# Performance work log

Hardware: AMD Instinct MI355X
Metric: run time of the kernel (lower is better)

Reference implementation:

```python
import jax, jax.numpy as jnp
import numpy as np

B, P, K = 32, 1024, 16  # clouds, points per cloud, neighbors


def setup_inputs() -> dict:
    key = jax.random.key(0)
    ks = jax.random.split(key, 5)
    N, C, H, D = B * P, 64, 128, 3
    x = jax.random.normal(ks[0], (N, C), dtype=jnp.float32)
    pos = jax.random.normal(ks[1], (N, D), dtype=jnp.float32)
    batch = jnp.arange(N, dtype=jnp.int64) // P  # cloud id per node
    W_e = jax.random.normal(ks[2], (2 * C, H), dtype=jnp.float32) * 0.05
    b_e = jnp.zeros((H,), dtype=jnp.float32)
    W_sc = jax.random.normal(ks[3], (C, H), dtype=jnp.float32) * 0.05
    b_sc = jnp.zeros((H,), dtype=jnp.float32)
    return {"x": x, "pos": pos, "batch": batch,
            "W_e": W_e, "b_e": b_e, "W_sc": W_sc, "b_sc": b_sc}


def _knn_idx(posb):
    # posb: [B, P, D] -> idx [B, P, K]: K nearest neighbors (sources) per target node,
    # within each cloud, excluding self (loop=False in torch_geometric.knn_graph).
    sq = jnp.sum(posb * posb, axis=-1)                       # [B, P]
    d2 = sq[:, :, None] + sq[:, None, :] - 2.0 * jnp.einsum('bid,bjd->bij', posb, posb)
    d2 = d2 + jnp.eye(P, dtype=posb.dtype)[None] * jnp.finfo(posb.dtype).max / 2
    _, idx = jax.lax.top_k(-d2, K)                           # [B, P, K]
    return idx


def reference(x, pos, batch, W_e, b_e, W_sc, b_sc):
    C = x.shape[-1]
    xb = x.reshape(B, P, C)
    posb = pos.reshape(B, P, -1)
    idx = _knn_idx(posb)                                     # [B, P, K]
    # gather neighbor (source) features per target node
    x_j = jax.vmap(lambda xc, ic: xc[ic])(xb, idx)           # [B, P, K, C]
    x_i = xb[:, :, None, :]                                  # [B, P, 1, C]
    # EdgeConv message: nn([x_i, x_j - x_i]), here Linear + ReLU
    e = jnp.concatenate([jnp.broadcast_to(x_i, x_j.shape), x_j - x_i], axis=-1)  # [B,P,K,2C]
    msg = jax.nn.relu(jnp.einsum('bpke,eh->bpkh', e, W_e) + b_e)
    agg = jnp.max(msg, axis=2)                               # max aggregation -> [B, P, H]
    shortcut = x @ W_sc + b_sc                               # [N, H]
    out = agg.reshape(-1, agg.shape[-1]) + shortcut
    return out
```

## Files before the change

kernel.cpp:

```cpp
#include <hip/hip_runtime.h>
#include <float.h>
#include <stdint.h>

#define BATCHES 32
#define P 1024
#define KNN 16
#define C 64
#define H 128
#define N (BATCHES * P)
#define SPLITS 8
#define CPS 128
#define QB 32
#define PADH 136

typedef short short8 __attribute__((ext_vector_type(8)));
typedef float floatx4 __attribute__((ext_vector_type(4)));

struct alignas(16) F4 { float x, y, z, w; };

__device__ __forceinline__ unsigned short f2bf(float f) {
    unsigned u = __float_as_uint(f);
    unsigned r = (u + 0x7FFF + ((u >> 16) & 1)) >> 16;
    return (unsigned short)r;
}

__global__ __launch_bounds__(256) void prep_kernel(
    const float* __restrict__ W_e, const float* __restrict__ b_e,
    const float* __restrict__ W_sc, const float* __restrict__ b_sc,
    const float* __restrict__ X,
    unsigned short* __restrict__ WT, float* __restrict__ bias,
    unsigned short* __restrict__ V)
{
    __shared__ unsigned short Vs[128][PADH];
    __shared__ unsigned short Wb[128 * 64];
    int b = blockIdx.x;
    int t = threadIdx.x;
    if (b < 96) {
        int i = b * 256 + t;
        int col = i >> 6, c = i & 63;
        float w;
        if (col < 128)      w = W_e[c * 128 + col] - W_e[(64 + c) * 128 + col];
        else if (col < 256) w = W_e[(64 + c) * 128 + (col - 128)];
        else                w = W_sc[c * 128 + (col - 256)];
        WT[col * 64 + c] = f2bf(w);
        if (c == 0) {
            bias[col] = (col < 128) ? b_e[col] : (col < 256 ? 0.0f : b_sc[col - 256]);
        }
        return;
    }

    int vb = b - 96;
    int m0 = vb * 128;
    int w  = t >> 6, ln = t & 63;
    int lm = ln & 15, kg = ln >> 4;

#pragma unroll 8
    for (int i = 0; i < 32; ++i) {
        int m = i * 256 + t;
        int k = m >> 7, h = m & 127;
        Wb[h * 64 + ((k + 8 * h) & 63)] = f2bf(W_e[(size_t)(64 + k) * 128 + h]);
    }

    short8 a0[2], a1[2];
#pragma unroll
    for (int i = 0; i < 2; ++i) {
        int row = m0 + (2 * w + i) * 16 + lm;
        const float4* ar = (const float4*)(X + (size_t)row * 64 + kg * 8);
        float4 f0 = ar[0], f1 = ar[1], f2 = ar[8], f3 = ar[9];
        a0[i][0] = (short)f2bf(f0.x); a0[i][1] = (short)f2bf(f0.y);
        a0[i][2] = (short)f2bf(f0.z); a0[i][3] = (short)f2bf(f0.w);
        a0[i][4] = (short)f2bf(f1.x); a0[i][5] = (short)f2bf(f1.y);
        a0[i][6] = (short)f2bf(f1.z); a0[i][7] = (short)f2bf(f1.w);
        a1[i][0] = (short)f2bf(f2.x); a1[i][1] = (short)f2bf(f2.y);
        a1[i][2] = (short)f2bf(f2.z); a1[i][3] = (short)f2bf(f2.w);
        a1[i][4] = (short)f2bf(f3.x); a1[i][5] = (short)f2bf(f3.y);
        a1[i][6] = (short)f2bf(f3.z); a1[i][7] = (short)f2bf(f3.w);
    }
    __syncthreads();

#pragma unroll 2
    for (int ct = 0; ct < 8; ++ct) {
        int col = ct * 16 + lm;
        int sbase = col * 64;
        short8 b0 = *(const short8*)&Wb[sbase + ((8 * (kg + col)) & 63)];
        short8 b1 = *(const short8*)&Wb[sbase + ((8 * (kg + col) + 32) & 63)];
#pragma unroll
        for (int i = 0; i < 2; ++i) {
            floatx4 acc = {0.0f, 0.0f, 0.0f, 0.0f};
            acc = __builtin_amdgcn_mfma_f32_16x16x32_bf16(a0[i], b0, acc, 0, 0, 0);
            acc = __builtin_amdgcn_mfma_f32_16x16x32_bf16(a1[i], b1, acc, 0, 0, 0);
#pragma unroll
            for (int r = 0; r < 4; ++r)
                Vs[(2 * w + i) * 16 + kg * 4 + r][col] = f2bf(acc[r]);
        }
    }
    __syncthreads();

    uint2* Vg = (uint2*)V + (size_t)vb * 4096;
#pragma unroll
    for (int i = t; i < 4096; i += 256) {
        int row = i >> 5, off = (i & 31) * 4;
        Vg[i] = *(const uint2*)&Vs[row][off];
    }
}

struct SM {
    F4 spos[P + 8];
    union {
        struct {
            float lists[SPLITS][16][QB];
            unsigned short offs[SPLITS][QB];
            unsigned short cnts[SPLITS][QB];
            float Tq[QB];
        };
        struct {
            unsigned short Ubuf[QB][PADH];
            unsigned short Sbuf[QB][PADH];
        };
    };
    int nbr[QB][KNN];
};

__global__ __launch_bounds__(256, 4) void knn_gemm_kernel(
    const float* __restrict__ pos, const float* __restrict__ X,
    const unsigned short* __restrict__ WT, const float* __restrict__ bias,
    const unsigned short* __restrict__ V,
    float* __restrict__ out)
{
    __shared__ __align__(16) SM A;

    int t = threadIdx.x;
    int q = t & 31, s = t >> 5;
    int blk = blockIdx.x;
    int batch = blk >> 5;
    int qblk  = blk & 31;
    int iloc  = qblk * QB + q;
    int so    = qblk >> 2;
    bool wave_owns = ((t >> 6) == (so >> 1));

    const float* pb = pos + (size_t)batch * P * 3;
    for (int j = t; j < P; j += 256) {
        float x = pb[j * 3 + 0], y = pb[j * 3 + 1], z = pb[j * 3 + 2];
        float sq = __fadd_rn(__fadd_rn(__fmul_rn(x, x), __fmul_rn(y, y)),
                             __fmul_rn(z, z));
        A.spos[j] = F4{x, y, z, sq};
    }
    __syncthreads();

    F4 me = A.spos[iloc];
    const int j0 = s * CPS;

    float d[16];
#pragma unroll
    for (int k = 0; k < 16; ++k) d[k] = FLT_MAX;

    auto dist_nc = [&](const F4& c) -> float {
        float dot = __fadd_rn(__fadd_rn(__fmul_rn(me.x, c.x), __fmul_rn(me.y, c.y)),
                              __fmul_rn(me.z, c.z));
        return __fadd_rn(__fadd_rn(me.w, c.w), __fmul_rn(-2.0f, dot));
    };
    auto dist = [&](const F4& c, int j) -> float {
        float d2 = dist_nc(c);
        return (j == iloc) ? FLT_MAX : d2;
    };
    auto insert = [&](float d2) {
#pragma unroll
        for (int k = 15; k >= 1; --k)
            d[k] = __builtin_amdgcn_fmed3f(d[k - 1], d2, d[k]);
        d[0] = fminf(d[0], d2);
    };

    if (wave_owns) {
#pragma unroll 8
        for (int jj = 0; jj < CPS; ++jj) {
            int j = j0 + jj;
            F4 c = A.spos[j];
            insert(dist(c, j));
        }
    } else {
#pragma unroll 8
        for (int jj = 0; jj < CPS; ++jj) {
            F4 c = A.spos[j0 + jj];
            insert(dist_nc(c));
        }
    }

#pragma unroll
    for (int k = 0; k < 16; ++k) A.lists[s][k][q] = d[k];
    __syncthreads();

    if ((t >> 6) == (blk & 3) && (t & 63) < QB) {
        int qm = t & 63;
        float v[8], wv[8];
        int   n[8];
#pragma unroll
        for (int l = 0; l < 8; ++l) {
            v[l]  = A.lists[l][0][qm];
            wv[l] = A.lists[l][1][qm];
            n[l]  = 0;
        }
        float T = 0.0f;
#pragma unroll 1
        for (int k = 0; k < 16; ++k) {
            float mn = fminf(fminf(fminf(v[0], v[1]), fminf(v[2], v[3])),
                             fminf(fminf(v[4], v[5]), fminf(v[6], v[7])));
            bool taken = false;
#pragma unroll
            for (int l = 0; l < 8; ++l) {
                bool tk = (!taken) && (v[l] == mn);
                taken = taken || tk;
                int ni = n[l] + (tk ? 1 : 0);
                int ri = ni + 1;
                float rv = A.lists[l][(ri < 16) ? ri : 15][qm];
                float wnew = (ri < 16) ? rv : FLT_MAX;
                v[l]  = tk ? wv[l] : v[l];
                wv[l] = tk ? wnew  : wv[l];
                n[l]  = ni;
            }
            T = mn;
        }
        A.Tq[qm] = T;
        int off = 0;
#pragma unroll
        for (int l = 0; l < 8; ++l) {
            A.offs[l][qm] = (unsigned short)off;
            A.cnts[l][qm] = (unsigned short)n[l];
            off += n[l];
        }
    }
    __syncthreads();

    {
        float T  = A.Tq[q];
        int   cap = A.cnts[s][q];
        int   ob  = A.offs[s][q];
        int   base = batch * P;
        int   cnt = 0;

        if (wave_owns) {
#pragma unroll 4
            for (int jj = 0; jj < CPS; ++jj) {
                int j = j0 + jj;
                F4 c = A.spos[j];
                float d2 = dist(c, j);
                if (d2 <= T && cnt < cap) {
                    A.nbr[q][ob + cnt] = base + j;
                    cnt++;
                }
            }
        } else {
#pragma unroll 4
            for (int jj = 0; jj < CPS; ++jj) {
                int j = j0 + jj;
                F4 c = A.spos[j];
                float d2 = dist_nc(c);
                if (d2 <= T && cnt < cap) {
                    A.nbr[q][ob + cnt] = base + j;
                    cnt++;
                }
            }
        }
    }
    __syncthreads();

    {
        int w  = t >> 6;
        int ln = t & 63;
        int mt = w & 1, nh = w >> 1;
        int m0 = blk * QB + mt * 16;
        int lm = ln & 15, kg = ln >> 4;

        const float4* arow = (const float4*)(X + (size_t)(m0 + lm) * 64 + kg * 8);
        float4 f0 = arow[0], f1 = arow[1];
        float4 f2 = arow[8], f3 = arow[9];
        short8 a0, a1;
        a0[0] = (short)f2bf(f0.x); a0[1] = (short)f2bf(f0.y);
        a0[2] = (short)f2bf(f0.z); a0[3] = (short)f2bf(f0.w);
        a0[4] = (short)f2bf(f1.x); a0[5] = (short)f2bf(f1.y);
        a0[6] = (short)f2bf(f1.z); a0[7] = (short)f2bf(f1.w);
        a1[0] = (short)f2bf(f2.x); a1[1] = (short)f2bf(f2.y);
        a1[2] = (short)f2bf(f2.z); a1[3] = (short)f2bf(f2.w);
        a1[4] = (short)f2bf(f3.x); a1[5] = (short)f2bf(f3.y);
        a1[6] = (short)f2bf(f3.z); a1[7] = (short)f2bf(f3.w);

        int tbase = (nh == 0) ? 0 : 16;
#pragma unroll 4
        for (int nt = tbase; nt < tbase + 8; ++nt) {
            const short8* brow = (const short8*)(WT + (size_t)(nt * 16 + lm) * 64 + kg * 8);
            short8 b0 = brow[0];
            short8 b1 = brow[4];
            floatx4 acc = {0.0f, 0.0f, 0.0f, 0.0f};
            acc = __builtin_amdgcn_mfma_f32_16x16x32_bf16(a0, b0, acc, 0, 0, 0);
            acc = __builtin_amdgcn_mfma_f32_16x16x32_bf16(a1, b1, acc, 0, 0, 0);

            int col = nt * 16 + lm;
            float bv = bias[col];
#pragma unroll
            for (int r = 0; r < 4; ++r) {
                int row = mt * 16 + kg * 4 + r;
                unsigned short val = f2bf(acc[r] + bv);
                if (col < 128) A.Ubuf[row][col] = val;
                else           A.Sbuf[row][col - 256] = val;
            }
        }
    }
    __syncthreads();

    {
        int pl = t >> 4;
        int c8 = t & 15;
#pragma unroll
        for (int half = 0; half < 2; ++half) {
            int q2 = half * 16 + pl;
            size_t p = (size_t)blk * QB + q2;

            uint4 uu = *(const uint4*)&A.Ubuf[q2][c8 * 8];
            uint4 ss = *(const uint4*)&A.Sbuf[q2][c8 * 8];

            float m0 = -FLT_MAX, m1 = -FLT_MAX, m2 = -FLT_MAX, m3 = -FLT_MAX;
            float m4 = -FLT_MAX, m5 = -FLT_MAX, m6 = -FLT_MAX, m7 = -FLT_MAX;
#pragma unroll
            for (int k = 0; k < KNN; ++k) {
                int row = A.nbr[q2][k];
                uint4 vv = *(const uint4*)(V + (size_t)row * H + c8 * 8);
                m0 = fmaxf(m0, __uint_as_float(vv.x << 16));
                m1 = fmaxf(m1, __uint_as_float(vv.x & 0xFFFF0000u));
                m2 = fmaxf(m2, __uint_as_float(vv.y << 16));
                m3 = fmaxf(m3, __uint_as_float(vv.y & 0xFFFF0000u));
                m4 = fmaxf(m4, __uint_as_float(vv.z << 16));
                m5 = fmaxf(m5, __uint_as_float(vv.z & 0xFFFF0000u));
                m6 = fmaxf(m6, __uint_as_float(vv.w << 16));
                m7 = fmaxf(m7, __uint_as_float(vv.w & 0xFFFF0000u));
            }

            float4 oa, ob;
            oa.x = fmaxf(__uint_as_float(uu.x << 16)         + m0, 0.0f) + __uint_as_float(ss.x << 16);
            oa.y = fmaxf(__uint_as_float(uu.x & 0xFFFF0000u) + m1, 0.0f) + __uint_as_float(ss.x & 0xFFFF0000u);
            oa.z = fmaxf(__uint_as_float(uu.y << 16)         + m2, 0.0f) + __uint_as_float(ss.y << 16);
            oa.w = fmaxf(__uint_as_float(uu.y & 0xFFFF0000u) + m3, 0.0f) + __uint_as_float(ss.y & 0xFFFF0000u);
            ob.x = fmaxf(__uint_as_float(uu.z << 16)         + m4, 0.0f) + __uint_as_float(ss.z << 16);
            ob.y = fmaxf(__uint_as_float(uu.z & 0xFFFF0000u) + m5, 0.0f) + __uint_as_float(ss.z & 0xFFFF0000u);
            ob.z = fmaxf(__uint_as_float(uu.w << 16)         + m6, 0.0f) + __uint_as_float(ss.w << 16);
            ob.w = fmaxf(__uint_as_float(uu.w & 0xFFFF0000u) + m7, 0.0f) + __uint_as_float(ss.w & 0xFFFF0000u);
            ((float4*)(out + p * H))[c8 * 2]     = oa;
            ((float4*)(out + p * H))[c8 * 2 + 1] = ob;
        }
    }
}

extern "C" void kernel_launch(void* const* d_in, const int* in_sizes, int n_in,
                              void* d_out, int out_size, void* d_ws, size_t ws_size,
                              hipStream_t stream)
{
    const float* x    = (const float*)d_in[0];
    const float* pos  = (const float*)d_in[1];
    const float* W_e  = (const float*)d_in[3];
    const float* b_e  = (const float*)d_in[4];
    const float* W_sc = (const float*)d_in[5];
    const float* b_sc = (const float*)d_in[6];
    float* out = (float*)d_out;

    char* ws = (char*)d_ws;
    const size_t OFF_V    = 0;
    const size_t OFF_WT   = 8ull << 20;
    const size_t OFF_BIAS = OFF_WT + 49152;

    unsigned short* V    = (unsigned short*)(ws + OFF_V);
    unsigned short* WT   = (unsigned short*)(ws + OFF_WT);
    float*          bias = (float*)(ws + OFF_BIAS);

    prep_kernel<<<96 + N / 128, 256, 0, stream>>>(W_e, b_e, W_sc, b_sc, x,
                                                  WT, bias, V);
    knn_gemm_kernel<<<N / QB, 256, 0, stream>>>(pos, x, WT, bias, V, out);
}
```

Measured before the change: 130.8 us.

## Fuse prep into kNN kernel and recompute neighbor GEMM on the fly

```diff
diff --git a/kernel.cpp b/kernel.cpp
--- a/kernel.cpp
+++ b/kernel.cpp
@@ -24,88 +24,11 @@
     return (unsigned short)r;
 }
 
-__global__ __launch_bounds__(256) void prep_kernel(
-    const float* __restrict__ W_e, const float* __restrict__ b_e,
-    const float* __restrict__ W_sc, const float* __restrict__ b_sc,
-    const float* __restrict__ X,
-    unsigned short* __restrict__ WT, float* __restrict__ bias,
-    unsigned short* __restrict__ V)
-{
-    __shared__ unsigned short Vs[128][PADH];
-    __shared__ unsigned short Wb[128 * 64];
-    int b = blockIdx.x;
-    int t = threadIdx.x;
-    if (b < 96) {
-        int i = b * 256 + t;
-        int col = i >> 6, c = i & 63;
-        float w;
-        if (col < 128)      w = W_e[c * 128 + col] - W_e[(64 + c) * 128 + col];
-        else if (col < 256) w = W_e[(64 + c) * 128 + (col - 128)];
-        else                w = W_sc[c * 128 + (col - 256)];
-        WT[col * 64 + c] = f2bf(w);
-        if (c == 0) {
-            bias[col] = (col < 128) ? b_e[col] : (col < 256 ? 0.0f : b_sc[col - 256]);
-        }
-        return;
-    }
-
-    int vb = b - 96;
-    int m0 = vb * 128;
-    int w  = t >> 6, ln = t & 63;
-    int lm = ln & 15, kg = ln >> 4;
-
-#pragma unroll 8
-    for (int i = 0; i < 32; ++i) {
-        int m = i * 256 + t;
-        int k = m >> 7, h = m & 127;
-        Wb[h * 64 + ((k + 8 * h) & 63)] = f2bf(W_e[(size_t)(64 + k) * 128 + h]);
-    }
-
-    short8 a0[2], a1[2];
-#pragma unroll
-    for (int i = 0; i < 2; ++i) {
-        int row = m0 + (2 * w + i) * 16 + lm;
-        const float4* ar = (const float4*)(X + (size_t)row * 64 + kg * 8);
-        float4 f0 = ar[0], f1 = ar[1], f2 = ar[8], f3 = ar[9];
-        a0[i][0] = (short)f2bf(f0.x); a0[i][1] = (short)f2bf(f0.y);
-        a0[i][2] = (short)f2bf(f0.z); a0[i][3] = (short)f2bf(f0.w);
-        a0[i][4] = (short)f2bf(f1.x); a0[i][5] = (short)f2bf(f1.y);
-        a0[i][6] = (short)f2bf(f1.z); a0[i][7] = (short)f2bf(f1.w);
-        a1[i][0] = (short)f2bf(f2.x); a1[i][1] = (short)f2bf(f2.y);
-        a1[i][2] = (short)f2bf(f2.z); a1[i][3] = (short)f2bf(f2.w);
-        a1[i][4] = (short)f2bf(f3.x); a1[i][5] = (short)f2bf(f3.y);
-        a1[i][6] = (short)f2bf(f3.z); a1[i][7] = (short)f2bf(f3.w);
-    }
-    __syncthreads();
-
-#pragma unroll 2
-    for (int ct = 0; ct < 8; ++ct) {
-        int col = ct * 16 + lm;
-        int sbase = col * 64;
-        short8 b0 = *(const short8*)&Wb[sbase + ((8 * (kg + col)) & 63)];
-        short8 b1 = *(const short8*)&Wb[sbase + ((8 * (kg + col) + 32) & 63)];
-#pragma unroll
-        for (int i = 0; i < 2; ++i) {
-            floatx4 acc = {0.0f, 0.0f, 0.0f, 0.0f};
-            acc = __builtin_amdgcn_mfma_f32_16x16x32_bf16(a0[i], b0, acc, 0, 0, 0);
-            acc = __builtin_amdgcn_mfma_f32_16x16x32_bf16(a1[i], b1, acc, 0, 0, 0);
-#pragma unroll
-            for (int r = 0; r < 4; ++r)
-                Vs[(2 * w + i) * 16 + kg * 4 + r][col] = f2bf(acc[r]);
-        }
-    }
-    __syncthreads();
-
-    uint2* Vg = (uint2*)V + (size_t)vb * 4096;
-#pragma unroll
-    for (int i = t; i < 4096; i += 256) {
-        int row = i >> 5, off = (i & 31) * 4;
-        Vg[i] = *(const uint2*)&Vs[row][off];
-    }
-}
-
 struct SM {
-    F4 spos[P + 8];
+    union {
+        F4 spos[P + 8];
+        unsigned short W2L[128 * 64];
+    };
     union {
         struct {
             float lists[SPLITS][16][QB];
@@ -121,10 +44,10 @@
     int nbr[QB][KNN];
 };
 
-__global__ __launch_bounds__(256, 4) void knn_gemm_kernel(
+__global__ __launch_bounds__(256, 4) void fused_kernel(
     const float* __restrict__ pos, const float* __restrict__ X,
-    const unsigned short* __restrict__ WT, const float* __restrict__ bias,
-    const unsigned short* __restrict__ V,
+    const float* __restrict__ W_e, const float* __restrict__ b_e,
+    const float* __restrict__ W_sc, const float* __restrict__ b_sc,
     float* __restrict__ out)
 {
     __shared__ __align__(16) SM A;
@@ -262,6 +185,13 @@
         }
     }
     __syncthreads();
+
+#pragma unroll 8
+    for (int i = t; i < 8192; i += 256) {
+        int k = i >> 7, h = i & 127;
+        float wv = W_e[(size_t)(64 + k) * 128 + h];
+        A.W2L[h * 64 + (((k >> 3) + h) & 7) * 8 + (k & 7)] = f2bf(wv);
+    }
 
     {
         int w  = t >> 6;
@@ -283,67 +213,86 @@
         a1[4] = (short)f2bf(f3.x); a1[5] = (short)f2bf(f3.y);
         a1[6] = (short)f2bf(f3.z); a1[7] = (short)f2bf(f3.w);
 
-        int tbase = (nh == 0) ? 0 : 16;
-#pragma unroll 4
-        for (int nt = tbase; nt < tbase + 8; ++nt) {
-            const short8* brow = (const short8*)(WT + (size_t)(nt * 16 + lm) * 64 + kg * 8);
-            short8 b0 = brow[0];
-            short8 b1 = brow[4];
+#pragma unroll 2
+        for (int nt = 0; nt < 8; ++nt) {
+            int col = nt * 16 + lm;
+            short8 b0, b1;
+            float bv;
+            if (nh == 0) {
+#pragma unroll
+                for (int i = 0; i < 8; ++i) {
+                    int c0 = kg * 8 + i, c1 = 32 + kg * 8 + i;
+                    b0[i] = (short)f2bf(W_e[(size_t)c0 * 128 + col]
+                                      - W_e[(size_t)(64 + c0) * 128 + col]);
+                    b1[i] = (short)f2bf(W_e[(size_t)c1 * 128 + col]
+                                      - W_e[(size_t)(64 + c1) * 128 + col]);
+                }
+                bv = b_e[col];
+            } else {
+#pragma unroll
+                for (int i = 0; i < 8; ++i) {
+                    b0[i] = (short)f2bf(W_sc[(size_t)(kg * 8 + i) * 128 + col]);
+                    b1[i] = (short)f2bf(W_sc[(size_t)(32 + kg * 8 + i) * 128 + col]);
+                }
+                bv = b_sc[col];
+            }
             floatx4 acc = {0.0f, 0.0f, 0.0f, 0.0f};
             acc = __builtin_amdgcn_mfma_f32_16x16x32_bf16(a0, b0, acc, 0, 0, 0);
             acc = __builtin_amdgcn_mfma_f32_16x16x32_bf16(a1, b1, acc, 0, 0, 0);
 
-            int col = nt * 16 + lm;
-            float bv = bias[col];
 #pragma unroll
             for (int r = 0; r < 4; ++r) {
                 int row = mt * 16 + kg * 4 + r;
                 unsigned short val = f2bf(acc[r] + bv);
-                if (col < 128) A.Ubuf[row][col] = val;
-                else           A.Sbuf[row][col - 256] = val;
+                if (nh == 0) A.Ubuf[row][col] = val;
+                else         A.Sbuf[row][col] = val;
             }
         }
     }
     __syncthreads();
 
     {
-        int pl = t >> 4;
-        int c8 = t & 15;
-#pragma unroll
-        for (int half = 0; half < 2; ++half) {
-            int q2 = half * 16 + pl;
-            size_t p = (size_t)blk * QB + q2;
-
-            uint4 uu = *(const uint4*)&A.Ubuf[q2][c8 * 8];
-            uint4 ss = *(const uint4*)&A.Sbuf[q2][c8 * 8];
-
-            float m0 = -FLT_MAX, m1 = -FLT_MAX, m2 = -FLT_MAX, m3 = -FLT_MAX;
-            float m4 = -FLT_MAX, m5 = -FLT_MAX, m6 = -FLT_MAX, m7 = -FLT_MAX;
-#pragma unroll
-            for (int k = 0; k < KNN; ++k) {
-                int row = A.nbr[q2][k];
-                uint4 vv = *(const uint4*)(V + (size_t)row * H + c8 * 8);
-                m0 = fmaxf(m0, __uint_as_float(vv.x << 16));
-                m1 = fmaxf(m1, __uint_as_float(vv.x & 0xFFFF0000u));
-                m2 = fmaxf(m2, __uint_as_float(vv.y << 16));
-                m3 = fmaxf(m3, __uint_as_float(vv.y & 0xFFFF0000u));
-                m4 = fmaxf(m4, __uint_as_float(vv.z << 16));
-                m5 = fmaxf(m5, __uint_as_float(vv.z & 0xFFFF0000u));
-                m6 = fmaxf(m6, __uint_as_float(vv.w << 16));
-                m7 = fmaxf(m7, __uint_as_float(vv.w & 0xFFFF0000u));
-            }
-
-            float4 oa, ob;
-            oa.x = fmaxf(__uint_as_float(uu.x << 16)         + m0, 0.0f) + __uint_as_float(ss.x << 16);
-            oa.y = fmaxf(__uint_as_float(uu.x & 0xFFFF0000u) + m1, 0.0f) + __uint_as_float(ss.x & 0xFFFF0000u);
-            oa.z = fmaxf(__uint_as_float(uu.y << 16)         + m2, 0.0f) + __uint_as_float(ss.y << 16);
-            oa.w = fmaxf(__uint_as_float(uu.y & 0xFFFF0000u) + m3, 0.0f) + __uint_as_float(ss.y & 0xFFFF0000u);
-            ob.x = fmaxf(__uint_as_float(uu.z << 16)         + m4, 0.0f) + __uint_as_float(ss.z << 16);
-            ob.y = fmaxf(__uint_as_float(uu.z & 0xFFFF0000u) + m5, 0.0f) + __uint_as_float(ss.z & 0xFFFF0000u);
-            ob.z = fmaxf(__uint_as_float(uu.w << 16)         + m6, 0.0f) + __uint_as_float(ss.w << 16);
-            ob.w = fmaxf(__uint_as_float(uu.w & 0xFFFF0000u) + m7, 0.0f) + __uint_as_float(ss.w & 0xFFFF0000u);
-            ((float4*)(out + p * H))[c8 * 2]     = oa;
-            ((float4*)(out + p * H))[c8 * 2 + 1] = ob;
+        int w  = t >> 6;
+        int ln = t & 63;
+        int lm = ln & 15, kg = ln >> 4;
+
+#pragma unroll 2
+        for (int qi = 0; qi < 8; ++qi) {
+            int qq = w * 8 + qi;
+            int nb = A.nbr[qq][lm];
+            const float4* xr = (const float4*)(X + (size_t)nb * 64 + kg * 8);
+            float4 f0 = xr[0], f1 = xr[1], f2 = xr[8], f3 = xr[9];
+            short8 a0, a1;
+            a0[0] = (short)f2bf(f0.x); a0[1] = (short)f2bf(f0.y);
+            a0[2] = (short)f2bf(f0.z); a0[3] = (short)f2bf(f0.w);
+            a0[4] = (short)f2bf(f1.x); a0[5] = (short)f2bf(f1.y);
+            a0[6] = (short)f2bf(f1.z); a0[7] = (short)f2bf(f1.w);
+            a1[0] = (short)f2bf(f2.x); a1[1] = (short)f2bf(f2.y);
+            a1[2] = (short)f2bf(f2.z); a1[3] = (short)f2bf(f2.w);
+            a1[4] = (short)f2bf(f3.x); a1[5] = (short)f2bf(f3.y);
+            a1[6] = (short)f2bf(f3.z); a1[7] = (short)f2bf(f3.w);
+
+            size_t orow = (size_t)(blk * QB + qq) * H;
+#pragma unroll
+            for (int ct = 0; ct < 8; ++ct) {
+                int col = ct * 16 + lm;
+                const short8* wrow = (const short8*)&A.W2L[col * 64];
+                short8 b0 = wrow[(kg + col) & 7];
+                short8 b1 = wrow[(kg + 4 + col) & 7];
+                floatx4 acc = {0.0f, 0.0f, 0.0f, 0.0f};
+                acc = __builtin_amdgcn_mfma_f32_16x16x32_bf16(a0, b0, acc, 0, 0, 0);
+                acc = __builtin_amdgcn_mfma_f32_16x16x32_bf16(a1, b1, acc, 0, 0, 0);
+
+                float m = fmaxf(fmaxf(acc[0], acc[1]), fmaxf(acc[2], acc[3]));
+                m = fmaxf(m, __shfl_xor(m, 16));
+                m = fmaxf(m, __shfl_xor(m, 32));
+
+                if (ln < 16) {
+                    float u  = __uint_as_float((unsigned)A.Ubuf[qq][col] << 16);
+                    float sv = __uint_as_float((unsigned)A.Sbuf[qq][col] << 16);
+                    out[orow + col] = fmaxf(u + m, 0.0f) + sv;
+                }
+            }
         }
     }
 }
@@ -360,16 +309,5 @@
     const float* b_sc = (const float*)d_in[6];
     float* out = (float*)d_out;
 
-    char* ws = (char*)d_ws;
-    const size_t OFF_V    = 0;
-    const size_t OFF_WT   = 8ull << 20;
-    const size_t OFF_BIAS = OFF_WT + 49152;
-
-    unsigned short* V    = (unsigned short*)(ws + OFF_V);
-    unsigned short* WT   = (unsigned short*)(ws + OFF_WT);
-    float*          bias = (float*)(ws + OFF_BIAS);
-
-    prep_kernel<<<96 + N / 128, 256, 0, stream>>>(W_e, b_e, W_sc, b_sc, x,
-                                                  WT, bias, V);
-    knn_gemm_kernel<<<N / QB, 256, 0, stream>>>(pos, x, WT, bias, V, out);
+    fused_kernel<<<N / QB, 256, 0, stream>>>(pos, x, W_e, b_e, W_sc, b_sc, out);
 }
```

Result: slower. 144.0 us (+10.1%).

## Move U and S projections into prep kernel, slim knn kernel

Applied to the files above, without the earlier changes.

```diff
diff --git a/kernel.cpp b/kernel.cpp
--- a/kernel.cpp
+++ b/kernel.cpp
@@ -28,38 +28,15 @@
     const float* __restrict__ W_e, const float* __restrict__ b_e,
     const float* __restrict__ W_sc, const float* __restrict__ b_sc,
     const float* __restrict__ X,
-    unsigned short* __restrict__ WT, float* __restrict__ bias,
-    unsigned short* __restrict__ V)
+    unsigned short* __restrict__ U, unsigned short* __restrict__ V,
+    unsigned short* __restrict__ S)
 {
     __shared__ unsigned short Vs[128][PADH];
-    __shared__ unsigned short Wb[128 * 64];
-    int b = blockIdx.x;
-    int t = threadIdx.x;
-    if (b < 96) {
-        int i = b * 256 + t;
-        int col = i >> 6, c = i & 63;
-        float w;
-        if (col < 128)      w = W_e[c * 128 + col] - W_e[(64 + c) * 128 + col];
-        else if (col < 256) w = W_e[(64 + c) * 128 + (col - 128)];
-        else                w = W_sc[c * 128 + (col - 256)];
-        WT[col * 64 + c] = f2bf(w);
-        if (c == 0) {
-            bias[col] = (col < 128) ? b_e[col] : (col < 256 ? 0.0f : b_sc[col - 256]);
-        }
-        return;
-    }
-
-    int vb = b - 96;
+    int vb = blockIdx.x;
+    int t  = threadIdx.x;
     int m0 = vb * 128;
     int w  = t >> 6, ln = t & 63;
     int lm = ln & 15, kg = ln >> 4;
-
-#pragma unroll 8
-    for (int i = 0; i < 32; ++i) {
-        int m = i * 256 + t;
-        int k = m >> 7, h = m & 127;
-        Wb[h * 64 + ((k + 8 * h) & 63)] = f2bf(W_e[(size_t)(64 + k) * 128 + h]);
-    }
 
     short8 a0[2], a1[2];
 #pragma unroll
@@ -76,55 +53,77 @@
         a1[i][4] = (short)f2bf(f3.x); a1[i][5] = (short)f2bf(f3.y);
         a1[i][6] = (short)f2bf(f3.z); a1[i][7] = (short)f2bf(f3.w);
     }
-    __syncthreads();
-
+
+#pragma unroll 1
+    for (int os = 0; os < 3; ++os) {
 #pragma unroll 2
-    for (int ct = 0; ct < 8; ++ct) {
-        int col = ct * 16 + lm;
-        int sbase = col * 64;
-        short8 b0 = *(const short8*)&Wb[sbase + ((8 * (kg + col)) & 63)];
-        short8 b1 = *(const short8*)&Wb[sbase + ((8 * (kg + col) + 32) & 63)];
-#pragma unroll
-        for (int i = 0; i < 2; ++i) {
-            floatx4 acc = {0.0f, 0.0f, 0.0f, 0.0f};
-            acc = __builtin_amdgcn_mfma_f32_16x16x32_bf16(a0[i], b0, acc, 0, 0, 0);
-            acc = __builtin_amdgcn_mfma_f32_16x16x32_bf16(a1[i], b1, acc, 0, 0, 0);
-#pragma unroll
-            for (int r = 0; r < 4; ++r)
-                Vs[(2 * w + i) * 16 + kg * 4 + r][col] = f2bf(acc[r]);
-        }
-    }
-    __syncthreads();
-
-    uint2* Vg = (uint2*)V + (size_t)vb * 4096;
-#pragma unroll
-    for (int i = t; i < 4096; i += 256) {
-        int row = i >> 5, off = (i & 31) * 4;
-        Vg[i] = *(const uint2*)&Vs[row][off];
+        for (int ct = 0; ct < 8; ++ct) {
+            int col = ct * 16 + lm;
+            short8 b0, b1;
+            float bv;
+            if (os == 0) {
+#pragma unroll
+                for (int i = 0; i < 8; ++i) {
+                    int c0 = kg * 8 + i, c1 = 32 + kg * 8 + i;
+                    b0[i] = (short)f2bf(W_e[(size_t)c0 * 128 + col]
+                                      - W_e[(size_t)(64 + c0) * 128 + col]);
+                    b1[i] = (short)f2bf(W_e[(size_t)c1 * 128 + col]
+                                      - W_e[(size_t)(64 + c1) * 128 + col]);
+                }
+                bv = b_e[col];
+            } else if (os == 1) {
+#pragma unroll
+                for (int i = 0; i < 8; ++i) {
+                    b0[i] = (short)f2bf(W_e[(size_t)(64 + kg * 8 + i) * 128 + col]);
+                    b1[i] = (short)f2bf(W_e[(size_t)(96 + kg * 8 + i) * 128 + col]);
+                }
+                bv = 0.0f;
+            } else {
+#pragma unroll
+                for (int i = 0; i < 8; ++i) {
+                    b0[i] = (short)f2bf(W_sc[(size_t)(kg * 8 + i) * 128 + col]);
+                    b1[i] = (short)f2bf(W_sc[(size_t)(32 + kg * 8 + i) * 128 + col]);
+                }
+                bv = b_sc[col];
+            }
+#pragma unroll
+            for (int i = 0; i < 2; ++i) {
+                floatx4 acc = {0.0f, 0.0f, 0.0f, 0.0f};
+                acc = __builtin_amdgcn_mfma_f32_16x16x32_bf16(a0[i], b0, acc, 0, 0, 0);
+                acc = __builtin_amdgcn_mfma_f32_16x16x32_bf16(a1[i], b1, acc, 0, 0, 0);
+#pragma unroll
+                for (int r = 0; r < 4; ++r)
+                    Vs[(2 * w + i) * 16 + kg * 4 + r][col] = f2bf(acc[r] + bv);
+            }
+        }
+        __syncthreads();
+
+        unsigned short* dst = (os == 0) ? U : (os == 1) ? V : S;
+        uint2* Dg = (uint2*)dst + (size_t)vb * 4096;
+#pragma unroll
+        for (int i = t; i < 4096; i += 256) {
+            int row = i >> 5, off = (i & 31) * 4;
+            Dg[i] = *(const uint2*)&Vs[row][off];
+        }
+        __syncthreads();
     }
 }
 
 struct SM {
     F4 spos[P + 8];
-    union {
-        struct {
-            float lists[SPLITS][16][QB];
-            unsigned short offs[SPLITS][QB];
-            unsigned short cnts[SPLITS][QB];
-            float Tq[QB];
-        };
-        struct {
-            unsigned short Ubuf[QB][PADH];
-            unsigned short Sbuf[QB][PADH];
-        };
+    struct {
+        float lists[SPLITS][16][QB];
+        unsigned short offs[SPLITS][QB];
+        unsigned short cnts[SPLITS][QB];
+        float Tq[QB];
     };
     int nbr[QB][KNN];
 };
 
-__global__ __launch_bounds__(256, 4) void knn_gemm_kernel(
-    const float* __restrict__ pos, const float* __restrict__ X,
-    const unsigned short* __restrict__ WT, const float* __restrict__ bias,
-    const unsigned short* __restrict__ V,
+__global__ __launch_bounds__(256, 4) void knn_kernel(
+    const float* __restrict__ pos,
+    const unsigned short* __restrict__ U, const unsigned short* __restrict__ V,
+    const unsigned short* __restrict__ S,
     float* __restrict__ out)
 {
     __shared__ __align__(16) SM A;
@@ -264,49 +263,6 @@
     __syncthreads();
 
     {
-        int w  = t >> 6;
-        int ln = t & 63;
-        int mt = w & 1, nh = w >> 1;
-        int m0 = blk * QB + mt * 16;
-        int lm = ln & 15, kg = ln >> 4;
-
-        const float4* arow = (const float4*)(X + (size_t)(m0 + lm) * 64 + kg * 8);
-        float4 f0 = arow[0], f1 = arow[1];
-        float4 f2 = arow[8], f3 = arow[9];
-        short8 a0, a1;
-        a0[0] = (short)f2bf(f0.x); a0[1] = (short)f2bf(f0.y);
-        a0[2] = (short)f2bf(f0.z); a0[3] = (short)f2bf(f0.w);
-        a0[4] = (short)f2bf(f1.x); a0[5] = (short)f2bf(f1.y);
-        a0[6] = (short)f2bf(f1.z); a0[7] = (short)f2bf(f1.w);
-        a1[0] = (short)f2bf(f2.x); a1[1] = (short)f2bf(f2.y);
-        a1[2] = (short)f2bf(f2.z); a1[3] = (short)f2bf(f2.w);
-        a1[4] = (short)f2bf(f3.x); a1[5] = (short)f2bf(f3.y);
-        a1[6] = (short)f2bf(f3.z); a1[7] = (short)f2bf(f3.w);
-
-        int tbase = (nh == 0) ? 0 : 16;
-#pragma unroll 4
-        for (int nt = tbase; nt < tbase + 8; ++nt) {
-            const short8* brow = (const short8*)(WT + (size_t)(nt * 16 + lm) * 64 + kg * 8);
-            short8 b0 = brow[0];
-            short8 b1 = brow[4];
-            floatx4 acc = {0.0f, 0.0f, 0.0f, 0.0f};
-            acc = __builtin_amdgcn_mfma_f32_16x16x32_bf16(a0, b0, acc, 0, 0, 0);
-            acc = __builtin_amdgcn_mfma_f32_16x16x32_bf16(a1, b1, acc, 0, 0, 0);
-
-            int col = nt * 16 + lm;
-            float bv = bias[col];
-#pragma unroll
-            for (int r = 0; r < 4; ++r) {
-                int row = mt * 16 + kg * 4 + r;
-                unsigned short val = f2bf(acc[r] + bv);
-                if (col < 128) A.Ubuf[row][col] = val;
-                else           A.Sbuf[row][col - 256] = val;
-            }
-        }
-    }
-    __syncthreads();
-
-    {
         int pl = t >> 4;
         int c8 = t & 15;
 #pragma unroll
@@ -314,8 +270,8 @@
             int q2 = half * 16 + pl;
             size_t p = (size_t)blk * QB + q2;
 
-            uint4 uu = *(const uint4*)&A.Ubuf[q2][c8 * 8];
-            uint4 ss = *(const uint4*)&A.Sbuf[q2][c8 * 8];
+            uint4 uu = ((const uint4*)(U + p * H))[c8];
+            uint4 ss = ((const uint4*)(S + p * H))[c8];
 
             float m0 = -FLT_MAX, m1 = -FLT_MAX, m2 = -FLT_MAX, m3 = -FLT_MAX;
             float m4 = -FLT_MAX, m5 = -FLT_MAX, m6 = -FLT_MAX, m7 = -FLT_MAX;
@@ -361,15 +317,14 @@
     float* out = (float*)d_out;
 
     char* ws = (char*)d_ws;
-    const size_t OFF_V    = 0;
-    const size_t OFF_WT   = 8ull << 20;
-    const size_t OFF_BIAS = OFF_WT + 49152;
-
-    unsigned short* V    = (unsigned short*)(ws + OFF_V);
-    unsigned short* WT   = (unsigned short*)(ws + OFF_WT);
-    float*          bias = (float*)(ws + OFF_BIAS);
-
-    prep_kernel<<<96 + N / 128, 256, 0, stream>>>(W_e, b_e, W_sc, b_sc, x,
-                                                  WT, bias, V);
-    knn_gemm_kernel<<<N / QB, 256, 0, stream>>>(pos, x, WT, bias, V, out);
+    const size_t OFF_U = 0;
+    const size_t OFF_V = 8ull << 20;
+    const size_t OFF_S = 16ull << 20;
+
+    unsigned short* U = (unsigned short*)(ws + OFF_U);
+    unsigned short* V = (unsigned short*)(ws + OFF_V);
+    unsigned short* S = (unsigned short*)(ws + OFF_S);
+
+    prep_kernel<<<N / 128, 256, 0, stream>>>(W_e, b_e, W_sc, b_sc, x, U, V, S);
+    knn_kernel<<<N / QB, 256, 0, stream>>>(pos, U, V, S, out);
 }
```

Result: slower. 136.6 us (+4.4%).
